# Kernel optimization log

Hardware: AMD Instinct MI355X
Metric: run time of the kernel (lower is better)

Reference implementation:

```python
import jax, jax.numpy as jnp
import numpy as np

K = 16  # kNN neighbors
R = 4   # upsampling ratio


def knn_idx(x, k):
    """Per-cloud kNN (self excluded). x: [B,N,C] -> idx [B,N,k] int32."""
    sq = jnp.sum(x * x, axis=-1)  # [B,N]
    d = sq[:, :, None] + sq[:, None, :] - 2.0 * jnp.einsum('bnc,bmc->bnm', x, x)
    n = x.shape[1]
    d = d + jnp.eye(n, dtype=x.dtype) * jnp.asarray(1e9, x.dtype)  # exclude self-loop
    _, idx = jax.lax.top_k(-d, k)  # k smallest distances
    return idx


def edge_conv(x, idx, W, b):
    """EdgeConv: mlp([x_i, x_j - x_i]) with max aggregation over neighbors.
    x: [B,N,C], idx: [B,N,k] -> [B,N,out]."""
    nbr = jax.vmap(lambda xb, ib: xb[ib])(x, idx)            # [B,N,k,C] gather
    ctr = jnp.broadcast_to(x[:, :, None, :], nbr.shape)
    e = jnp.concatenate([ctr, nbr - ctr], axis=-1)           # [B,N,k,2C]
    h = jax.nn.relu(jnp.einsum('bnkc,cd->bnkd', e, W) + b)
    return jnp.max(h, axis=2)                                # max aggregate


def setup_inputs() -> dict:
    key = jax.random.key(0)
    ks = jax.random.split(key, 16)
    B, N = 8, 2048
    chans = [3, 32, 32, 64]  # DynConv stack: 3->32->32->64
    C = chans[-1]

    def lin(k, fan_in, fan_out):
        s = 1.0 / np.sqrt(fan_in)
        return jax.random.uniform(k, (fan_in, fan_out), jnp.float32, -s, s)

    inp = {'x': jax.random.normal(ks[0], (B, N, 3), jnp.float32)}
    # DynConv (EdgeConv) weights: Linear(2*in, out)
    for i in range(3):
        inp[f'W{i}'] = lin(ks[1 + i], 2 * chans[i], chans[i + 1])
        inp[f'b{i}'] = jnp.zeros((chans[i + 1],), jnp.float32)
    # NodeShuffle: EdgeConv(C -> R*C) then shuffle N -> N*R
    inp['Wup'] = lin(ks[5], 2 * C, R * C)
    inp['bup'] = jnp.zeros((R * C,), jnp.float32)
    # Reconstructor MLP([64,128,64,3])
    rdims = [64, 128, 64, 3]
    for i in range(3):
        inp[f'Wr{i}'] = lin(ks[6 + i], rdims[i], rdims[i + 1])
        inp[f'br{i}'] = jnp.zeros((rdims[i + 1],), jnp.float32)
    return inp


def reference(x, W0, b0, W1, b1, W2, b2, Wup, bup, Wr0, br0, Wr1, br1, Wr2, br2):
    # Dynamic feature extractor: recompute kNN on current feature space each layer
    for W, b in ((W0, b0), (W1, b1), (W2, b2)):
        idx = knn_idx(x, K)
        x = edge_conv(x, idx, W, b)
    # NodeShuffle upsampler: EdgeConv to R*C channels, then shuffle nodes
    idx = knn_idx(x, K)
    h = edge_conv(x, idx, Wup, bup)              # [B,N,R*C]
    B, N, _ = h.shape
    C = h.shape[-1] // R
    x = h.reshape(B, N, R, C).reshape(B, N * R, C)  # [B,N*R,C]
    # Reconstructor MLP -> xyz
    x = jax.nn.relu(x @ Wr0 + br0)
    x = jax.nn.relu(x @ Wr1 + br1)
    return x @ Wr2 + br2                          # [B,N*R,3]
```

## Files before the change

kernel.cpp:

```cpp
#include <hip/hip_runtime.h>

#define B_ 8
#define N_ 2048
#define K_ 16
#define M_ (B_*N_)

__device__ __forceinline__ unsigned long long kmin(unsigned long long a, unsigned long long b) {
    return a < b ? a : b;
}

template<int C>
__global__ __launch_bounds__(256, 2) void knn_kernel(const float* __restrict__ X,
                                                     int* __restrict__ idx_out) {
    constexpr int ROWS = 32, TPR = 8, TJ = 128;
    constexpr int SJ = (C == 3) ? 4 : (C + 4);
    __shared__ float xj[TJ * SJ];

    int tid = threadIdx.x;
    int rlocal = tid / TPR;
    int r = tid & (TPR - 1);
    int m = blockIdx.x * ROWS + rlocal;
    int b = m >> 11;
    int i = m & (N_ - 1);

    const float* xrow = X + (size_t)m * C;
    float xi[C];
#pragma unroll
    for (int c = 0; c < C; ++c) xi[c] = xrow[c];

    unsigned long long t[16];
#pragma unroll
    for (int q = 0; q < 16; ++q) t[q] = ~0ull;

    const float* Xb = X + (size_t)b * N_ * C;

    for (int jt = 0; jt < N_ / TJ; ++jt) {
        __syncthreads();
        if constexpr (C == 3) {
            for (int e = tid; e < TJ * 3; e += 256)
                xj[(e / 3) * 4 + (e % 3)] = Xb[jt * TJ * 3 + e];
        } else {
            constexpr int C4 = C / 4;
            const float4* src = (const float4*)(Xb + (size_t)jt * TJ * C);
            for (int e4 = tid; e4 < TJ * C4; e4 += 256) {
                int jl = e4 / C4, c4 = e4 % C4;
                *(float4*)&xj[jl * SJ + c4 * 4] = src[e4];
            }
        }
        __syncthreads();

#pragma unroll 2
        for (int jl = r; jl < TJ; jl += TPR) {
            float s = 0.f;
            if constexpr (C == 3) {
#pragma unroll
                for (int c = 0; c < 3; ++c) {
                    float df = xi[c] - xj[jl * SJ + c];
                    s = fmaf(df, df, s);
                }
            } else {
#pragma unroll
                for (int c4 = 0; c4 < C / 4; ++c4) {
                    float4 v = *(const float4*)&xj[jl * SJ + c4 * 4];
                    float d0 = xi[c4 * 4 + 0] - v.x;
                    float d1 = xi[c4 * 4 + 1] - v.y;
                    float d2 = xi[c4 * 4 + 2] - v.z;
                    float d3 = xi[c4 * 4 + 3] - v.w;
                    s = fmaf(d0, d0, s);
                    s = fmaf(d1, d1, s);
                    s = fmaf(d2, d2, s);
                    s = fmaf(d3, d3, s);
                }
            }
            int jg = jt * TJ + jl;
            unsigned u = __float_as_uint(s);
            u ^= (unsigned)(((int)u >> 31) | 0x80000000);
            unsigned long long key = ((unsigned long long)u << 32) | (unsigned)jg;
            if (jg == i) key = ~0ull;
            if (key < t[15]) {
                t[15] = key;
#pragma unroll
                for (int s2 = 15; s2 > 0; --s2) {
                    unsigned long long a = t[s2 - 1], bb = t[s2];
                    bool sw = bb < a;
                    t[s2 - 1] = sw ? bb : a;
                    t[s2]     = sw ? a : bb;
                }
            }
        }
    }

#pragma unroll
    for (int msk = 1; msk <= 4; msk <<= 1) {
        unsigned long long o[16];
#pragma unroll
        for (int q = 0; q < 16; ++q)
            o[q] = __shfl_xor((unsigned long long)t[q], msk, 64);
        unsigned long long nt[16];
#pragma unroll
        for (int q = 0; q < 16; ++q) nt[q] = kmin(t[q], o[15 - q]);
#pragma unroll
        for (int s2 = 8; s2 >= 1; s2 >>= 1) {
#pragma unroll
            for (int q = 0; q < 16; ++q) {
                if (!(q & s2)) {
                    unsigned long long a = nt[q], bb = nt[q | s2];
                    bool sw = bb < a;
                    nt[q]      = sw ? bb : a;
                    nt[q | s2] = sw ? a : bb;
                }
            }
        }
#pragma unroll
        for (int q = 0; q < 16; ++q) t[q] = nt[q];
    }

    if (r == 0) {
        int* op = idx_out + (size_t)m * K_;
#pragma unroll
        for (int q = 0; q < 16; ++q) op[q] = (int)(unsigned)(t[q] & 0xffffffffull);
    }
}

template<int C, int D>
__global__ __launch_bounds__(256) void t1_kernel(const float* __restrict__ X,
                                                 const float* __restrict__ W,
                                                 double* __restrict__ T1) {
    constexpr int D4 = D / 4;
    int e4 = blockIdx.x * 256 + threadIdx.x;
    if (e4 >= M_ * D4) return;
    int m = e4 / D4, d4 = e4 - m * D4;
    const float* xr = X + (size_t)m * C;
    double a0 = 0.0, a1 = 0.0, a2 = 0.0, a3 = 0.0;
#pragma unroll
    for (int c = 0; c < C; ++c) {
        double a = (double)xr[c];
        float4 w = *(const float4*)&W[(size_t)c * D + d4 * 4];
        a0 = fma(a, (double)w.x, a0);
        a1 = fma(a, (double)w.y, a1);
        a2 = fma(a, (double)w.z, a2);
        a3 = fma(a, (double)w.w, a3);
    }
    double* op = &T1[(size_t)e4 * 4];
    op[0] = a0; op[1] = a1; op[2] = a2; op[3] = a3;
}

template<int C, int D, int TN>
__global__ __launch_bounds__(256) void gemm_max_kernel(
        const float* __restrict__ X, const double* __restrict__ T1,
        const float* __restrict__ W, const float* __restrict__ bias,
        const int* __restrict__ idx, float* __restrict__ O) {
    constexpr int CS  = (C == 3) ? 4 : C + 4;
    constexpr int LPR = TN / 4;
    constexpr int TW  = 256 / TN;
    constexpr int UR  = TN / 16;
    __shared__ float Xs[64 * CS];
    __shared__ float Ws[C * TN];
    __shared__ float Xi[4 * CS];
    __shared__ int   idxs[64];

    int tid = threadIdx.x;
    int m0p = blockIdx.x * 4;
    int n0  = blockIdx.y * TN;
    int b   = m0p >> 11;
    const float* Xb = X + ((size_t)b << 11) * C;
    const float* Wb = W + (size_t)C * D;

    if (tid < 64) idxs[tid] = idx[(size_t)m0p * K_ + tid];
    if (tid < 4 * C) {
        int pl = tid / C, c = tid - pl * C;
        Xi[pl * CS + c] = X[(size_t)(m0p + pl) * C + c];
    }
    __syncthreads();

    if constexpr (C == 3) {
        for (int e = tid; e < 64 * 3; e += 256) {
            int r = e / 3, c = e - r * 3;
            int j = idxs[r];
            Xs[r * CS + c] = Xb[(size_t)j * 3 + c] - Xi[(r >> 4) * CS + c];
        }
    } else {
        constexpr int C4 = C / 4;
        for (int e4 = tid; e4 < 64 * C4; e4 += 256) {
            int r = e4 / C4, c4 = e4 - r * C4;
            int j = idxs[r];
            float4 v  = *(const float4*)&Xb[(size_t)j * C + c4 * 4];
            float4 xc = *(const float4*)&Xi[(r >> 4) * CS + c4 * 4];
            v.x -= xc.x; v.y -= xc.y; v.z -= xc.z; v.w -= xc.w;
            *(float4*)&Xs[r * CS + c4 * 4] = v;
        }
    }
    for (int e = tid; e < C * TN; e += 256) {
        int cr = e / TN;
        Ws[e] = Wb[(size_t)cr * D + n0 + (e - cr * TN)];
    }
    __syncthreads();

    int tx = tid % LPR, ty = tid / LPR;
    int m = m0p + ty / TW;

    const double* t1p = &T1[(size_t)m * D + n0 + tx * 4];
    double t10 = t1p[0], t11 = t1p[1], t12 = t1p[2], t13 = t1p[3];
    double acc[UR][4];
#pragma unroll
    for (int u = 0; u < UR; ++u) {
        acc[u][0] = t10; acc[u][1] = t11; acc[u][2] = t12; acc[u][3] = t13;
    }

#pragma unroll 2
    for (int c = 0; c < C; ++c) {
        float4 w = *(const float4*)&Ws[c * TN + tx * 4];
        double w0 = (double)w.x, w1 = (double)w.y, w2 = (double)w.z, w3 = (double)w.w;
#pragma unroll
        for (int u = 0; u < UR; ++u) {
            double a = (double)Xs[(ty * UR + u) * CS + c];
            acc[u][0] = fma(a, w0, acc[u][0]);
            acc[u][1] = fma(a, w1, acc[u][1]);
            acc[u][2] = fma(a, w2, acc[u][2]);
            acc[u][3] = fma(a, w3, acc[u][3]);
        }
    }

    double bm[4];
#pragma unroll
    for (int q = 0; q < 4; ++q) bm[q] = acc[0][q];
#pragma unroll
    for (int u = 1; u < UR; ++u)
#pragma unroll
        for (int q = 0; q < 4; ++q) bm[q] = fmax(bm[q], acc[u][q]);

#pragma unroll
    for (int off = LPR; off < LPR * TW; off <<= 1)
#pragma unroll
        for (int q = 0; q < 4; ++q)
            bm[q] = fmax(bm[q], __shfl_xor(bm[q], off, 64));

    if (ty % TW == 0) {
        float4 bi = *(const float4*)&bias[n0 + tx * 4];
        float4 o;
        o.x = (float)fmax(bm[0] + (double)bi.x, 0.0);
        o.y = (float)fmax(bm[1] + (double)bi.y, 0.0);
        o.z = (float)fmax(bm[2] + (double)bi.z, 0.0);
        o.w = (float)fmax(bm[3] + (double)bi.w, 0.0);
        *(float4*)&O[(size_t)m * D + n0 + tx * 4] = o;
    }
}

__global__ __launch_bounds__(256) void recon_kernel(const float* __restrict__ U,
        const float* __restrict__ W0, const float* __restrict__ b0,
        const float* __restrict__ W1, const float* __restrict__ b1,
        const float* __restrict__ W2, const float* __restrict__ b2,
        float* __restrict__ O) {
    __shared__ float F[32 * 68];
    __shared__ float H1[128 * 33];
    __shared__ float H2[64 * 33];
    __shared__ float W2s[64 * 4];
    __shared__ float b0s[128], b1s[64], b2s[4];

    int tid = threadIdx.x;
    int m0 = blockIdx.x * 32;

    {
        const float4* src = (const float4*)(U + (size_t)m0 * 64);
        for (int e4 = tid; e4 < 32 * 16; e4 += 256) {
            int p = e4 >> 4, c4 = e4 & 15;
            *(float4*)&F[p * 68 + c4 * 4] = src[e4];
        }
    }
    if (tid < 192) W2s[(tid / 3) * 4 + (tid % 3)] = W2[tid];
    if (tid < 128) b0s[tid] = b0[tid];
    else if (tid < 192) b1s[tid - 128] = b1[tid - 128];
    else if (tid == 192) { b2s[0] = b2[0]; b2s[1] = b2[1]; b2s[2] = b2[2]; }
    __syncthreads();

    int p = tid >> 3, s = tid & 7;

    float acc[16];
#pragma unroll
    for (int q = 0; q < 16; ++q) acc[q] = 0.f;
    for (int c = 0; c < 64; ++c) {
        float a = F[p * 68 + c];
#pragma unroll
        for (int q = 0; q < 4; ++q) {
            float4 w = *(const float4*)&W0[c * 128 + s * 4 + q * 32];
            acc[q * 4 + 0] = fmaf(a, w.x, acc[q * 4 + 0]);
            acc[q * 4 + 1] = fmaf(a, w.y, acc[q * 4 + 1]);
            acc[q * 4 + 2] = fmaf(a, w.z, acc[q * 4 + 2]);
            acc[q * 4 + 3] = fmaf(a, w.w, acc[q * 4 + 3]);
        }
    }
#pragma unroll
    for (int q = 0; q < 4; ++q)
#pragma unroll
        for (int i2 = 0; i2 < 4; ++i2) {
            int dd = s * 4 + q * 32 + i2;
            H1[dd * 33 + p] = fmaxf(acc[q * 4 + i2] + b0s[dd], 0.f);
        }
    __syncthreads();

    float a2[8];
#pragma unroll
    for (int q = 0; q < 8; ++q) a2[q] = 0.f;
    for (int c = 0; c < 128; ++c) {
        float a = H1[c * 33 + p];
#pragma unroll
        for (int q = 0; q < 2; ++q) {
            float4 w = *(const float4*)&W1[c * 64 + s * 4 + q * 32];
            a2[q * 4 + 0] = fmaf(a, w.x, a2[q * 4 + 0]);
            a2[q * 4 + 1] = fmaf(a, w.y, a2[q * 4 + 1]);
            a2[q * 4 + 2] = fmaf(a, w.z, a2[q * 4 + 2]);
            a2[q * 4 + 3] = fmaf(a, w.w, a2[q * 4 + 3]);
        }
    }
#pragma unroll
    for (int q = 0; q < 2; ++q)
#pragma unroll
        for (int i2 = 0; i2 < 4; ++i2) {
            int dd = s * 4 + q * 32 + i2;
            H2[dd * 33 + p] = fmaxf(a2[q * 4 + i2] + b1s[dd], 0.f);
        }
    __syncthreads();

    if (tid < 96) {
        int p3 = tid / 3, d3 = tid - p3 * 3;
        float av = 0.f;
#pragma unroll
        for (int c = 0; c < 64; ++c)
            av = fmaf(H2[c * 33 + p3], W2s[c * 4 + d3], av);
        O[(size_t)(m0 + p3) * 3 + d3] = av + b2s[d3];
    }
}

extern "C" void kernel_launch(void* const* d_in, const int* in_sizes, int n_in,
                              void* d_out, int out_size, void* d_ws, size_t ws_size,
                              hipStream_t stream) {
    const float* x   = (const float*)d_in[0];
    const float* W0  = (const float*)d_in[1];
    const float* b0  = (const float*)d_in[2];
    const float* W1  = (const float*)d_in[3];
    const float* b1  = (const float*)d_in[4];
    const float* W2  = (const float*)d_in[5];
    const float* b2  = (const float*)d_in[6];
    const float* Wup = (const float*)d_in[7];
    const float* bup = (const float*)d_in[8];
    const float* Wr0 = (const float*)d_in[9];
    const float* br0 = (const float*)d_in[10];
    const float* Wr1 = (const float*)d_in[11];
    const float* br1 = (const float*)d_in[12];
    const float* Wr2 = (const float*)d_in[13];
    const float* br2 = (const float*)d_in[14];
    float* out = (float*)d_out;

    char* ws = (char*)d_ws;
    size_t o = 0;
    auto alloc = [&](size_t nbytes) {
        void* pp = ws + o;
        o += (nbytes + 255) & ~(size_t)255;
        return pp;
    };
    float*  X1  = (float*)alloc((size_t)M_ * 32 * 4);
    float*  X2  = (float*)alloc((size_t)M_ * 32 * 4);
    float*  X3  = (float*)alloc((size_t)M_ * 64 * 4);
    double* T1  = (double*)alloc((size_t)M_ * 256 * 8);
    float*  H   = (float*)alloc((size_t)M_ * 256 * 4);
    int*    idxb = (int*)alloc((size_t)M_ * 16 * 4);

    knn_kernel<3><<<512, 256, 0, stream>>>(x, idxb);
    t1_kernel<3, 32><<<M_ * 8 / 256, 256, 0, stream>>>(x, W0, T1);
    gemm_max_kernel<3, 32, 32><<<dim3(M_ / 4, 1), 256, 0, stream>>>(x, T1, W0, b0, idxb, X1);
    knn_kernel<32><<<512, 256, 0, stream>>>(X1, idxb);
    t1_kernel<32, 32><<<M_ * 8 / 256, 256, 0, stream>>>(X1, W1, T1);
    gemm_max_kernel<32, 32, 32><<<dim3(M_ / 4, 1), 256, 0, stream>>>(X1, T1, W1, b1, idxb, X2);
    knn_kernel<32><<<512, 256, 0, stream>>>(X2, idxb);
    t1_kernel<32, 64><<<M_ * 16 / 256, 256, 0, stream>>>(X2, W2, T1);
    gemm_max_kernel<32, 64, 64><<<dim3(M_ / 4, 1), 256, 0, stream>>>(X2, T1, W2, b2, idxb, X3);
    knn_kernel<64><<<512, 256, 0, stream>>>(X3, idxb);
    t1_kernel<64, 256><<<M_ * 64 / 256, 256, 0, stream>>>(X3, Wup, T1);
    gemm_max_kernel<64, 256, 64><<<dim3(M_ / 4, 4), 256, 0, stream>>>(X3, T1, Wup, bup, idxb, H);
    recon_kernel<<<2048, 256, 0, stream>>>(H, Wr0, br0, Wr1, br1, Wr2, br2, out);
}
```

Measured before the change: 1.299 ms.

## Fuse center-term GEMM into edge kernel, loop N tiles, use fp32 for upsampler

Removes the separate t1_kernel and its double-precision T1 buffer by computing the center-point projection inside the edge kernel for each output tile. The edge kernel now loops over all output column tiles in one block, so the gathered neighbor features are reused across tiles. The last EdgeConv (64->256) accumulates in float instead of double, and block indices are swizzled across batches in both kNN and edge kernels. The fp32 path and the extra per-tile syncs trade some accuracy and serialization for less global traffic and less FP64 work.

```diff
diff --git a/kernel.cpp b/kernel.cpp
--- a/kernel.cpp
+++ b/kernel.cpp
@@ -8,6 +8,10 @@
 __device__ __forceinline__ unsigned long long kmin(unsigned long long a, unsigned long long b) {
     return a < b ? a : b;
 }
+__device__ __forceinline__ float  ffma(float a, float b, float c)  { return fmaf(a, b, c); }
+__device__ __forceinline__ double ffma(double a, double b, double c){ return fma(a, b, c); }
+__device__ __forceinline__ float  fmx(float a, float b)  { return fmaxf(a, b); }
+__device__ __forceinline__ double fmx(double a, double b){ return fmax(a, b); }
 
 template<int C>
 __global__ __launch_bounds__(256, 2) void knn_kernel(const float* __restrict__ X,
@@ -19,7 +23,8 @@
     int tid = threadIdx.x;
     int rlocal = tid / TPR;
     int r = tid & (TPR - 1);
-    int m = blockIdx.x * ROWS + rlocal;
+    int sb = (blockIdx.x & 7) * (M_ / ROWS / 8) + (blockIdx.x >> 3);
+    int m = sb * ROWS + rlocal;
     int b = m >> 11;
     int i = m & (N_ - 1);
 
@@ -122,49 +127,27 @@
     }
 }
 
-template<int C, int D>
-__global__ __launch_bounds__(256) void t1_kernel(const float* __restrict__ X,
-                                                 const float* __restrict__ W,
-                                                 double* __restrict__ T1) {
-    constexpr int D4 = D / 4;
-    int e4 = blockIdx.x * 256 + threadIdx.x;
-    if (e4 >= M_ * D4) return;
-    int m = e4 / D4, d4 = e4 - m * D4;
-    const float* xr = X + (size_t)m * C;
-    double a0 = 0.0, a1 = 0.0, a2 = 0.0, a3 = 0.0;
-#pragma unroll
-    for (int c = 0; c < C; ++c) {
-        double a = (double)xr[c];
-        float4 w = *(const float4*)&W[(size_t)c * D + d4 * 4];
-        a0 = fma(a, (double)w.x, a0);
-        a1 = fma(a, (double)w.y, a1);
-        a2 = fma(a, (double)w.z, a2);
-        a3 = fma(a, (double)w.w, a3);
-    }
-    double* op = &T1[(size_t)e4 * 4];
-    op[0] = a0; op[1] = a1; op[2] = a2; op[3] = a3;
-}
-
-template<int C, int D, int TN>
-__global__ __launch_bounds__(256) void gemm_max_kernel(
-        const float* __restrict__ X, const double* __restrict__ T1,
-        const float* __restrict__ W, const float* __restrict__ bias,
-        const int* __restrict__ idx, float* __restrict__ O) {
+template<int C, int D, int TN, typename ACC>
+__global__ __launch_bounds__(256) void edge_kernel(
+        const float* __restrict__ X, const float* __restrict__ W,
+        const float* __restrict__ bias, const int* __restrict__ idx,
+        float* __restrict__ O) {
+    constexpr int NTILE = D / TN;
     constexpr int CS  = (C == 3) ? 4 : C + 4;
     constexpr int LPR = TN / 4;
     constexpr int TW  = 256 / TN;
     constexpr int UR  = TN / 16;
+    constexpr int TN4 = TN / 4;
     __shared__ float Xs[64 * CS];
-    __shared__ float Ws[C * TN];
     __shared__ float Xi[4 * CS];
+    __shared__ float Ws[2 * C * TN];
     __shared__ int   idxs[64];
 
     int tid = threadIdx.x;
-    int m0p = blockIdx.x * 4;
-    int n0  = blockIdx.y * TN;
+    int sb  = (blockIdx.x & 7) * (M_ / 4 / 8) + (blockIdx.x >> 3);
+    int m0p = sb * 4;
     int b   = m0p >> 11;
     const float* Xb = X + ((size_t)b << 11) * C;
-    const float* Wb = W + (size_t)C * D;
 
     if (tid < 64) idxs[tid] = idx[(size_t)m0p * K_ + tid];
     if (tid < 4 * C) {
@@ -190,59 +173,97 @@
             *(float4*)&Xs[r * CS + c4 * 4] = v;
         }
     }
-    for (int e = tid; e < C * TN; e += 256) {
-        int cr = e / TN;
-        Ws[e] = Wb[(size_t)cr * D + n0 + (e - cr * TN)];
-    }
-    __syncthreads();
 
     int tx = tid % LPR, ty = tid / LPR;
-    int m = m0p + ty / TW;
-
-    const double* t1p = &T1[(size_t)m * D + n0 + tx * 4];
-    double t10 = t1p[0], t11 = t1p[1], t12 = t1p[2], t13 = t1p[3];
-    double acc[UR][4];
-#pragma unroll
-    for (int u = 0; u < UR; ++u) {
-        acc[u][0] = t10; acc[u][1] = t11; acc[u][2] = t12; acc[u][3] = t13;
-    }
-
+    int p  = ty / TW;
+    int m  = m0p + p;
+
+    for (int t = 0; t < NTILE; ++t) {
+        int n0 = t * TN;
+        for (int e4 = tid; e4 < 2 * C * TN4; e4 += 256) {
+            int rr = e4 / TN4, j4 = e4 - rr * TN4;
+            *(float4*)&Ws[rr * TN + j4 * 4] = *(const float4*)&W[(size_t)rr * D + n0 + j4 * 4];
+        }
+        __syncthreads();
+
+        ACC s0 = 0, s1 = 0, s2 = 0, s3 = 0;
+#pragma unroll 4
+        for (int c = 0; c < C; ++c) {
+            ACC a = (ACC)Xi[p * CS + c];
+            float4 w = *(const float4*)&Ws[c * TN + tx * 4];
+            s0 = ffma(a, (ACC)w.x, s0);
+            s1 = ffma(a, (ACC)w.y, s1);
+            s2 = ffma(a, (ACC)w.z, s2);
+            s3 = ffma(a, (ACC)w.w, s3);
+        }
+        ACC acc[UR][4];
+#pragma unroll
+        for (int u = 0; u < UR; ++u) {
+            acc[u][0] = s0; acc[u][1] = s1; acc[u][2] = s2; acc[u][3] = s3;
+        }
+
+        if constexpr (C == 3) {
+#pragma unroll
+            for (int c = 0; c < 3; ++c) {
+                float4 w = *(const float4*)&Ws[(3 + c) * TN + tx * 4];
+                ACC w0 = (ACC)w.x, w1 = (ACC)w.y, w2 = (ACC)w.z, w3 = (ACC)w.w;
+#pragma unroll
+                for (int u = 0; u < UR; ++u) {
+                    ACC a = (ACC)Xs[(ty * UR + u) * CS + c];
+                    acc[u][0] = ffma(a, w0, acc[u][0]);
+                    acc[u][1] = ffma(a, w1, acc[u][1]);
+                    acc[u][2] = ffma(a, w2, acc[u][2]);
+                    acc[u][3] = ffma(a, w3, acc[u][3]);
+                }
+            }
+        } else {
 #pragma unroll 2
-    for (int c = 0; c < C; ++c) {
-        float4 w = *(const float4*)&Ws[c * TN + tx * 4];
-        double w0 = (double)w.x, w1 = (double)w.y, w2 = (double)w.z, w3 = (double)w.w;
-#pragma unroll
-        for (int u = 0; u < UR; ++u) {
-            double a = (double)Xs[(ty * UR + u) * CS + c];
-            acc[u][0] = fma(a, w0, acc[u][0]);
-            acc[u][1] = fma(a, w1, acc[u][1]);
-            acc[u][2] = fma(a, w2, acc[u][2]);
-            acc[u][3] = fma(a, w3, acc[u][3]);
-        }
-    }
-
-    double bm[4];
-#pragma unroll
-    for (int q = 0; q < 4; ++q) bm[q] = acc[0][q];
-#pragma unroll
-    for (int u = 1; u < UR; ++u)
-#pragma unroll
-        for (int q = 0; q < 4; ++q) bm[q] = fmax(bm[q], acc[u][q]);
-
-#pragma unroll
-    for (int off = LPR; off < LPR * TW; off <<= 1)
-#pragma unroll
-        for (int q = 0; q < 4; ++q)
-            bm[q] = fmax(bm[q], __shfl_xor(bm[q], off, 64));
-
-    if (ty % TW == 0) {
-        float4 bi = *(const float4*)&bias[n0 + tx * 4];
-        float4 o;
-        o.x = (float)fmax(bm[0] + (double)bi.x, 0.0);
-        o.y = (float)fmax(bm[1] + (double)bi.y, 0.0);
-        o.z = (float)fmax(bm[2] + (double)bi.z, 0.0);
-        o.w = (float)fmax(bm[3] + (double)bi.w, 0.0);
-        *(float4*)&O[(size_t)m * D + n0 + tx * 4] = o;
+            for (int c4 = 0; c4 < C / 4; ++c4) {
+                float4 xv[UR];
+#pragma unroll
+                for (int u = 0; u < UR; ++u)
+                    xv[u] = *(const float4*)&Xs[(ty * UR + u) * CS + c4 * 4];
+#pragma unroll
+                for (int cc = 0; cc < 4; ++cc) {
+                    float4 w = *(const float4*)&Ws[(C + c4 * 4 + cc) * TN + tx * 4];
+                    ACC w0 = (ACC)w.x, w1 = (ACC)w.y, w2 = (ACC)w.z, w3 = (ACC)w.w;
+#pragma unroll
+                    for (int u = 0; u < UR; ++u) {
+                        float av = (cc == 0) ? xv[u].x : (cc == 1) ? xv[u].y
+                                 : (cc == 2) ? xv[u].z : xv[u].w;
+                        ACC a = (ACC)av;
+                        acc[u][0] = ffma(a, w0, acc[u][0]);
+                        acc[u][1] = ffma(a, w1, acc[u][1]);
+                        acc[u][2] = ffma(a, w2, acc[u][2]);
+                        acc[u][3] = ffma(a, w3, acc[u][3]);
+                    }
+                }
+            }
+        }
+
+        ACC bm[4];
+#pragma unroll
+        for (int q = 0; q < 4; ++q) bm[q] = acc[0][q];
+#pragma unroll
+        for (int u = 1; u < UR; ++u)
+#pragma unroll
+            for (int q = 0; q < 4; ++q) bm[q] = fmx(bm[q], acc[u][q]);
+#pragma unroll
+        for (int off = LPR; off < LPR * TW; off <<= 1)
+#pragma unroll
+            for (int q = 0; q < 4; ++q)
+                bm[q] = fmx(bm[q], (ACC)__shfl_xor(bm[q], off, 64));
+
+        if (ty % TW == 0) {
+            float4 bi = *(const float4*)&bias[n0 + tx * 4];
+            float4 o;
+            o.x = (float)fmx(bm[0] + (ACC)bi.x, (ACC)0);
+            o.y = (float)fmx(bm[1] + (ACC)bi.y, (ACC)0);
+            o.z = (float)fmx(bm[2] + (ACC)bi.z, (ACC)0);
+            o.w = (float)fmx(bm[3] + (ACC)bi.w, (ACC)0);
+            *(float4*)&O[(size_t)m * D + n0 + tx * 4] = o;
+        }
+        __syncthreads();
     }
 }
 
@@ -358,24 +379,19 @@
         o += (nbytes + 255) & ~(size_t)255;
         return pp;
     };
-    float*  X1  = (float*)alloc((size_t)M_ * 32 * 4);
-    float*  X2  = (float*)alloc((size_t)M_ * 32 * 4);
-    float*  X3  = (float*)alloc((size_t)M_ * 64 * 4);
-    double* T1  = (double*)alloc((size_t)M_ * 256 * 8);
-    float*  H   = (float*)alloc((size_t)M_ * 256 * 4);
-    int*    idxb = (int*)alloc((size_t)M_ * 16 * 4);
+    float* X1   = (float*)alloc((size_t)M_ * 32 * 4);
+    float* X2   = (float*)alloc((size_t)M_ * 32 * 4);
+    float* X3   = (float*)alloc((size_t)M_ * 64 * 4);
+    float* H    = (float*)alloc((size_t)M_ * 256 * 4);
+    int*   idxb = (int*)alloc((size_t)M_ * 16 * 4);
 
     knn_kernel<3><<<512, 256, 0, stream>>>(x, idxb);
-    t1_kernel<3, 32><<<M_ * 8 / 256, 256, 0, stream>>>(x, W0, T1);
-    gemm_max_kernel<3, 32, 32><<<dim3(M_ / 4, 1), 256, 0, stream>>>(x, T1, W0, b0, idxb, X1);
+    edge_kernel<3, 32, 32, double><<<M_ / 4, 256, 0, stream>>>(x, W0, b0, idxb, X1);
     knn_kernel<32><<<512, 256, 0, stream>>>(X1, idxb);
-    t1_kernel<32, 32><<<M_ * 8 / 256, 256, 0, stream>>>(X1, W1, T1);
-    gemm_max_kernel<32, 32, 32><<<dim3(M_ / 4, 1), 256, 0, stream>>>(X1, T1, W1, b1, idxb, X2);
+    edge_kernel<32, 32, 32, double><<<M_ / 4, 256, 0, stream>>>(X1, W1, b1, idxb, X2);
     knn_kernel<32><<<512, 256, 0, stream>>>(X2, idxb);
-    t1_kernel<32, 64><<<M_ * 16 / 256, 256, 0, stream>>>(X2, W2, T1);
-    gemm_max_kernel<32, 64, 64><<<dim3(M_ / 4, 1), 256, 0, stream>>>(X2, T1, W2, b2, idxb, X3);
+    edge_kernel<32, 64, 64, double><<<M_ / 4, 256, 0, stream>>>(X2, W2, b2, idxb, X3);
     knn_kernel<64><<<512, 256, 0, stream>>>(X3, idxb);
-    t1_kernel<64, 256><<<M_ * 64 / 256, 256, 0, stream>>>(X3, Wup, T1);
-    gemm_max_kernel<64, 256, 64><<<dim3(M_ / 4, 4), 256, 0, stream>>>(X3, T1, Wup, bup, idxb, H);
+    edge_kernel<64, 256, 64, float><<<M_ / 4, 256, 0, stream>>>(X3, Wup, bup, idxb, H);
     recon_kernel<<<2048, 256, 0, stream>>>(H, Wr0, br0, Wr1, br1, Wr2, br2, out);
 }
```

After: 1.155 ms. -11.1%, faster.
